# Kernel tuning notes

Hardware: AMD Instinct MI355X
Metric: run time of the kernel (lower is better)

## Reference

```python
import jax, jax.numpy as jnp
import numpy as np

D_MODEL = 1024
D_FEATURE = 64
B, S = 4, 4096


def setup_inputs() -> dict:
    key = jax.random.key(0)
    ks = jax.random.split(key, 9)
    s = 1.0 / np.sqrt(D_MODEL)
    return {
        "queries": jax.random.normal(ks[0], (B, S, D_MODEL), jnp.float32),
        "keys": jax.random.normal(ks[1], (B, S, D_MODEL), jnp.float32),
        "values": jax.random.normal(ks[2], (B, S, D_MODEL), jnp.float32),
        "Wq": jax.random.uniform(ks[3], (D_FEATURE, D_MODEL), jnp.float32, -s, s),
        "bq": jax.random.uniform(ks[4], (D_FEATURE,), jnp.float32, -s, s),
        "Wk": jax.random.uniform(ks[5], (D_FEATURE, D_MODEL), jnp.float32, -s, s),
        "bk": jax.random.uniform(ks[6], (D_FEATURE,), jnp.float32, -s, s),
        "Wv": jax.random.uniform(ks[7], (D_FEATURE, D_MODEL), jnp.float32, -s, s),
        "bv": jax.random.uniform(ks[8], (D_FEATURE,), jnp.float32, -s, s),
    }


def reference(queries, keys, values, Wq, bq, Wk, bk, Wv, bv):
    # Linear projections: x @ W.T + b
    q = jnp.einsum("bsm,fm->bsf", queries, Wq) + bq   # [B,S,Df]
    k = jnp.einsum("bsm,fm->bsf", keys, Wk) + bk
    v = jnp.einsum("bsm,fm->bsf", values, Wv) + bv
    d_k = k.shape[-1]
    # Full NxN score matrix (faithful to the naive bmm implementation)
    attn = jnp.einsum("bqf,bkf->bqk", q, k) / jnp.sqrt(jnp.float32(d_k))
    attn = jax.nn.softmax(attn, axis=2)
    # dropout is identity in eval mode; mask is never forwarded in the original
    out = jnp.einsum("bqk,bkf->bqf", attn, v)  # [B,S,Df]
    return out
```

## Files before the change

### kernel.cpp

```cpp
#include <hip/hip_runtime.h>

#define NB 4
#define SEQ 4096
#define DM 1024
#define DF 64

typedef unsigned short u16;
typedef unsigned int u32;
typedef __attribute__((ext_vector_type(8))) _Float16 half8;
typedef __attribute__((ext_vector_type(8))) unsigned short ushort8;
typedef __attribute__((ext_vector_type(4))) float f32x4;

__device__ __forceinline__ u16 f2h(float f) {
    union { _Float16 h; u16 u; } v; v.h = (_Float16)f; return v.u;
}

#define MFMAH(a, b, c) __builtin_amdgcn_mfma_f32_16x16x32_f16(a, b, c, 0, 0, 0)

__global__ __launch_bounds__(256) void wprep_kernel(
    const float* __restrict__ W0, const float* __restrict__ W1, const float* __restrict__ W2,
    u16* __restrict__ Wh)
{
    int i = blockIdx.x * 256 + threadIdx.x;
    const float* W = (i < 65536) ? W0 : (i < 131072) ? W1 : W2;
    Wh[i] = f2h(W[i & 65535]);
}

#define KST 72
__global__ __launch_bounds__(256) void proj5_kernel(
    const float* __restrict__ X0, const float* __restrict__ X1, const float* __restrict__ X2,
    const u16* __restrict__ Wh,
    const float* __restrict__ b0, const float* __restrict__ b1, const float* __restrict__ b2,
    u16* __restrict__ Oall)
{
    __shared__ u16 xs[64 * KST];
    __shared__ u16 ws[64 * KST];

    const int t    = threadIdx.x;
    const int w    = t >> 6;
    const int lane = t & 63;
    const int m15  = lane & 15;
    const int quad = lane >> 4;
    const int y    = blockIdx.y;

    const float* X    = (y == 0) ? X0 : (y == 1) ? X1 : X2;
    const float* bias = (y == 0) ? b0 : (y == 1) ? b1 : b2;
    const u16*   wp   = Wh + y * 65536;
    u16*         O    = Oall + (size_t)y * (NB * SEQ * DF);

    const long r0 = (long)blockIdx.x * 64;

    const int xrow = t >> 4;
    const int xc4  = t & 15;
    const int wrow = t >> 3;
    const int wc8  = t & 7;

    f32x4 acc[4];
#pragma unroll
    for (int F = 0; F < 4; ++F) acc[F] = (f32x4){0.f, 0.f, 0.f, 0.f};

    float4  xr[4];
    ushort8 wr[2];
#pragma unroll
    for (int i = 0; i < 4; ++i)
        xr[i] = *(const float4*)(X + (r0 + xrow + 16 * i) * DM + 4 * xc4);
#pragma unroll
    for (int i = 0; i < 2; ++i)
        wr[i] = *(const ushort8*)(wp + (wrow + 32 * i) * DM + 8 * wc8);

    for (int s = 0; s < 16; ++s) {
        __syncthreads();
#pragma unroll
        for (int i = 0; i < 4; ++i) {
            const int row = xrow + 16 * i;
            ushort4 h;
            h.x = f2h(xr[i].x); h.y = f2h(xr[i].y);
            h.z = f2h(xr[i].z); h.w = f2h(xr[i].w);
            *(ushort4*)&xs[row * KST + 4 * xc4] = h;
        }
#pragma unroll
        for (int i = 0; i < 2; ++i)
            *(ushort8*)&ws[(wrow + 32 * i) * KST + 8 * wc8] = wr[i];
        __syncthreads();

        if (s + 1 < 16) {
            const int k1 = 64 * (s + 1);
#pragma unroll
            for (int i = 0; i < 4; ++i)
                xr[i] = *(const float4*)(X + (r0 + xrow + 16 * i) * DM + k1 + 4 * xc4);
#pragma unroll
            for (int i = 0; i < 2; ++i)
                wr[i] = *(const ushort8*)(wp + (wrow + 32 * i) * DM + k1 + 8 * wc8);
        }

        const u16* ax = &xs[(16 * w + m15) * KST + quad * 8];
        half8 a0 = *(const half8*)ax;
        half8 a1 = *(const half8*)(ax + 32);
#pragma unroll
        for (int F = 0; F < 4; ++F) {
            const u16* bx = &ws[(16 * F + m15) * KST + quad * 8];
            half8 b0 = *(const half8*)bx;
            half8 b1 = *(const half8*)(bx + 32);
            acc[F] = MFMAH(a0, b0, acc[F]);
            acc[F] = MFMAH(a1, b1, acc[F]);
        }
    }

#pragma unroll
    for (int F = 0; F < 4; ++F) {
        float bv = bias[16 * F + m15];
#pragma unroll
        for (int r = 0; r < 4; ++r)
            O[(r0 + 16 * w + 4 * quad + r) * DF + 16 * F + m15] = f2h(acc[F][r] + bv);
    }
}

#define KSTR 72

__global__ __launch_bounds__(256) void attn_mfma_kernel(
    const u16* __restrict__ Qg, const u16* __restrict__ Kg, const u16* __restrict__ Vg,
    float* __restrict__ Opart, float* __restrict__ Mp, float* __restrict__ Lp,
    int ntiles, int norm)
{
    __shared__ u16 ks[64 * KSTR];
    __shared__ u16 vt[64 * KSTR];
    __shared__ u16 ps[4][16 * KSTR];

    const int t    = threadIdx.x;
    const int w    = t >> 6;
    const int lane = t & 63;
    const int m15  = lane & 15;
    const int quad = lane >> 4;
    const int b    = blockIdx.y;
    const int z    = blockIdx.z;
    const int q0   = blockIdx.x * 64;

    const u16* qptr = Qg + ((long)(b * SEQ + q0 + 16 * w + m15)) * DF + quad * 8;
    half8 qa0 = *(const half8*)qptr;
    half8 qa1 = *(const half8*)(qptr + 32);

    f32x4 accO[4];
#pragma unroll
    for (int F = 0; F < 4; ++F) accO[F] = (f32x4){0.f, 0.f, 0.f, 0.f};
    float mrow[4] = {-1e30f, -1e30f, -1e30f, -1e30f};
    float lrow[4] = {0.f, 0.f, 0.f, 0.f};

    const long kvbase = ((long)b * SEQ + (long)z * ntiles * 64) * DF;
    const ushort4* kb4 = (const ushort4*)(Kg + kvbase);
    const ushort4* vb4 = (const ushort4*)(Vg + kvbase);

    ushort4 kreg[4], vreg[4];
    const int krow  = t >> 4;
    const int kcol4 = t & 15;
    const int vj0   = (t & 15) * 4;
    const int vf0   = (t >> 4) * 4;
#pragma unroll
    for (int c = 0; c < 4; ++c) {
        kreg[c] = kb4[(krow + 16 * c) * 16 + kcol4];
        vreg[c] = vb4[(vj0 + c) * 16 + (vf0 >> 2)];
    }

    for (int tile = 0; tile < ntiles; ++tile) {
        __syncthreads();
#pragma unroll
        for (int c = 0; c < 4; ++c)
            *(ushort4*)&ks[(krow + 16 * c) * KSTR + kcol4 * 4] = kreg[c];
        {
            ushort4 w0 = {vreg[0].x, vreg[1].x, vreg[2].x, vreg[3].x};
            ushort4 w1 = {vreg[0].y, vreg[1].y, vreg[2].y, vreg[3].y};
            ushort4 w2 = {vreg[0].z, vreg[1].z, vreg[2].z, vreg[3].z};
            ushort4 w3 = {vreg[0].w, vreg[1].w, vreg[2].w, vreg[3].w};
            *(ushort4*)&vt[(vf0 + 0) * KSTR + vj0] = w0;
            *(ushort4*)&vt[(vf0 + 1) * KSTR + vj0] = w1;
            *(ushort4*)&vt[(vf0 + 2) * KSTR + vj0] = w2;
            *(ushort4*)&vt[(vf0 + 3) * KSTR + vj0] = w3;
        }
        __syncthreads();

        if (tile + 1 < ntiles) {
#pragma unroll
            for (int c = 0; c < 4; ++c) {
                kreg[c] = kb4[(tile + 1) * 1024 + (krow + 16 * c) * 16 + kcol4];
                vreg[c] = vb4[(tile + 1) * 1024 + (vj0 + c) * 16 + (vf0 >> 2)];
            }
        }

        f32x4 S[4];
#pragma unroll
        for (int T = 0; T < 4; ++T) {
            const u16* kp = &ks[(16 * T + m15) * KSTR + quad * 8];
            half8 kb0 = *(const half8*)kp;
            half8 kb1 = *(const half8*)(kp + 32);
            S[T] = MFMAH(qa0, kb0, ((f32x4){0.f, 0.f, 0.f, 0.f}));
            S[T] = MFMAH(qa1, kb1, S[T]);
        }

        float mx[4], alpha[4], mn[4], psum[4];
#pragma unroll
        for (int T = 0; T < 4; ++T)
#pragma unroll
            for (int r = 0; r < 4; ++r) S[T][r] *= 0.125f;
#pragma unroll
        for (int r = 0; r < 4; ++r) {
            mx[r] = fmaxf(fmaxf(S[0][r], S[1][r]), fmaxf(S[2][r], S[3][r]));
#pragma unroll
            for (int s = 1; s < 16; s <<= 1) mx[r] = fmaxf(mx[r], __shfl_xor(mx[r], s));
            mn[r] = fmaxf(mrow[r], mx[r]);
            alpha[r] = __expf(mrow[r] - mn[r]);
            mrow[r] = mn[r];
            psum[r] = 0.f;
        }
#pragma unroll
        for (int T = 0; T < 4; ++T)
#pragma unroll
            for (int r = 0; r < 4; ++r) {
                float p = __expf(S[T][r] - mn[r]);
                psum[r] += p;
                ps[w][(4 * quad + r) * KSTR + 16 * T + m15] = f2h(p);
            }
#pragma unroll
        for (int r = 0; r < 4; ++r) {
#pragma unroll
            for (int s = 1; s < 16; s <<= 1) psum[r] += __shfl_xor(psum[r], s);
            lrow[r] = lrow[r] * alpha[r] + psum[r];
        }
#pragma unroll
        for (int F = 0; F < 4; ++F)
#pragma unroll
            for (int r = 0; r < 4; ++r) accO[F][r] *= alpha[r];

        const u16* pp = &ps[w][m15 * KSTR + quad * 8];
        half8 pa0 = *(const half8*)pp;
        half8 pa1 = *(const half8*)(pp + 32);
#pragma unroll
        for (int F = 0; F < 4; ++F) {
            const u16* vp = &vt[(16 * F + m15) * KSTR + quad * 8];
            half8 vb0 = *(const half8*)vp;
            half8 vb1 = *(const half8*)(vp + 32);
            accO[F] = MFMAH(pa0, vb0, accO[F]);
            accO[F] = MFMAH(pa1, vb1, accO[F]);
        }
    }

    const long rowbase = (long)b * SEQ + q0 + 16 * w;
    if (norm) {
        float il[4];
#pragma unroll
        for (int r = 0; r < 4; ++r) il[r] = 1.f / lrow[r];
#pragma unroll
        for (int F = 0; F < 4; ++F)
#pragma unroll
            for (int r = 0; r < 4; ++r)
                Opart[(rowbase + 4 * quad + r) * DF + 16 * F + m15] = accO[F][r] * il[r];
    } else {
        float* Og = Opart + (size_t)z * (NB * SEQ * DF);
#pragma unroll
        for (int F = 0; F < 4; ++F)
#pragma unroll
            for (int r = 0; r < 4; ++r)
                Og[(rowbase + 4 * quad + r) * DF + 16 * F + m15] = accO[F][r];
        if (m15 == 0) {
#pragma unroll
            for (int r = 0; r < 4; ++r) {
                long rg = (long)z * (NB * SEQ) + rowbase + 4 * quad + r;
                Mp[rg] = mrow[r];
                Lp[rg] = lrow[r];
            }
        }
    }
}

__global__ __launch_bounds__(256) void combine_kernel(
    const float* __restrict__ Opart, const float* __restrict__ Mp, const float* __restrict__ Lp,
    float* __restrict__ out, int nsplit)
{
    const int tg  = blockIdx.x * 256 + threadIdx.x;
    const int row = tg >> 2;
    const int f0  = (tg & 3) * 16;

    float m = -1e30f;
    for (int g = 0; g < nsplit; ++g) m = fmaxf(m, Mp[g * (NB * SEQ) + row]);

    float l = 0.f;
    float4 o[4];
#pragma unroll
    for (int i = 0; i < 4; ++i) o[i] = (float4){0.f, 0.f, 0.f, 0.f};

    for (int g = 0; g < nsplit; ++g) {
        float e = __expf(Mp[g * (NB * SEQ) + row] - m);
        l += Lp[g * (NB * SEQ) + row] * e;
        const float* Op = Opart + ((long)g * (NB * SEQ) + row) * DF + f0;
#pragma unroll
        for (int i = 0; i < 4; ++i) {
            float4 v = *(const float4*)(Op + 4 * i);
            o[i].x += v.x * e; o[i].y += v.y * e; o[i].z += v.z * e; o[i].w += v.w * e;
        }
    }
    const float inv = 1.f / l;
#pragma unroll
    for (int i = 0; i < 4; ++i) {
        float4 v = {o[i].x * inv, o[i].y * inv, o[i].z * inv, o[i].w * inv};
        *(float4*)(out + (long)row * DF + f0 + 4 * i) = v;
    }
}

extern "C" void kernel_launch(void* const* d_in, const int* in_sizes, int n_in,
                              void* d_out, int out_size, void* d_ws, size_t ws_size,
                              hipStream_t stream) {
    (void)in_sizes; (void)n_in; (void)out_size;

    const float* X[3]  = { (const float*)d_in[0], (const float*)d_in[1], (const float*)d_in[2] };
    const float* W[3]  = { (const float*)d_in[3], (const float*)d_in[5], (const float*)d_in[7] };
    const float* Bv[3] = { (const float*)d_in[4], (const float*)d_in[6], (const float*)d_in[8] };

    char* wsb = (char*)d_ws;
    const size_t P_BYTES  = (size_t)3 * NB * SEQ * DF * 2;
    const size_t WH_BYTES = (size_t)3 * DF * DM * 2;
    const size_t ML_BYTES = (size_t)4 * NB * SEQ * 4;
    const size_t OP_BYTES = (size_t)NB * SEQ * DF * 4;

    u16*   P   = (u16*)wsb;
    u16*   Wh  = (u16*)(wsb + P_BYTES);
    float* Mp  = (float*)(wsb + P_BYTES + WH_BYTES);
    float* Lp  = (float*)(wsb + P_BYTES + WH_BYTES + ML_BYTES);
    float* Op  = (float*)(wsb + P_BYTES + WH_BYTES + 2 * ML_BYTES);
    const size_t base_need = P_BYTES + WH_BYTES + 2 * ML_BYTES;

    int nsplit = 1;
    if (ws_size >= base_need + 4 * OP_BYTES)      nsplit = 4;
    else if (ws_size >= base_need + 2 * OP_BYTES) nsplit = 2;
    const int ntiles = (SEQ / 64) / nsplit;

    float* out = (float*)d_out;

    wprep_kernel<<<768, 256, 0, stream>>>(W[0], W[1], W[2], Wh);

    dim3 pgrid(NB * SEQ / 64, 3);
    proj5_kernel<<<pgrid, 256, 0, stream>>>(X[0], X[1], X[2], Wh,
                                            Bv[0], Bv[1], Bv[2], P);

    const size_t proj_elems = (size_t)NB * SEQ * DF;
    dim3 agrid(SEQ / 64, NB, nsplit);
    if (nsplit == 1) {
        attn_mfma_kernel<<<agrid, 256, 0, stream>>>(P, P + proj_elems, P + 2 * proj_elems,
                                                    out, Mp, Lp, ntiles, 1);
    } else {
        attn_mfma_kernel<<<agrid, 256, 0, stream>>>(P, P + proj_elems, P + 2 * proj_elems,
                                                    Op, Mp, Lp, ntiles, 0);
        combine_kernel<<<(NB * SEQ * 4) / 256, 256, 0, stream>>>(Op, Mp, Lp, out, nsplit);
    }
}
```

Before: 281.7 us.

## Double-buffer projection LDS tiles and split output features across 512 threads

The projection kernel now uses two shared-memory buffers for the X and W tiles and prefetches two stages ahead, which drops one barrier per k-step. It also doubles the block to 512 threads, so eight waves split the 64 output features into two halves and each wave holds fewer accumulators. The goal is more memory parallelism and better latency hiding on what is a bandwidth-bound read of the three fp32 inputs. In exchange it doubles LDS per block and adds a launch-bounds occupancy hint that may constrain registers.

```diff
diff --git a/kernel.cpp b/kernel.cpp
--- a/kernel.cpp
+++ b/kernel.cpp
@@ -27,20 +27,22 @@
 }
 
 #define KST 72
-__global__ __launch_bounds__(256) void proj5_kernel(
+__global__ __launch_bounds__(512, 6) void proj6_kernel(
     const float* __restrict__ X0, const float* __restrict__ X1, const float* __restrict__ X2,
     const u16* __restrict__ Wh,
     const float* __restrict__ b0, const float* __restrict__ b1, const float* __restrict__ b2,
     u16* __restrict__ Oall)
 {
-    __shared__ u16 xs[64 * KST];
-    __shared__ u16 ws[64 * KST];
+    __shared__ u16 xs[2][64 * KST];
+    __shared__ u16 wt[2][64 * KST];
 
     const int t    = threadIdx.x;
     const int w    = t >> 6;
     const int lane = t & 63;
     const int m15  = lane & 15;
     const int quad = lane >> 4;
+    const int wr   = w & 3;
+    const int wf   = w >> 2;
     const int y    = blockIdx.y;
 
     const float* X    = (y == 0) ? X0 : (y == 1) ? X1 : X2;
@@ -50,68 +52,74 @@
 
     const long r0 = (long)blockIdx.x * 64;
 
-    const int xrow = t >> 4;
-    const int xc4  = t & 15;
-    const int wrow = t >> 3;
-    const int wc8  = t & 7;
-
-    f32x4 acc[4];
-#pragma unroll
-    for (int F = 0; F < 4; ++F) acc[F] = (f32x4){0.f, 0.f, 0.f, 0.f};
-
-    float4  xr[4];
-    ushort8 wr[2];
-#pragma unroll
-    for (int i = 0; i < 4; ++i)
-        xr[i] = *(const float4*)(X + (r0 + xrow + 16 * i) * DM + 4 * xc4);
-#pragma unroll
-    for (int i = 0; i < 2; ++i)
-        wr[i] = *(const ushort8*)(wp + (wrow + 32 * i) * DM + 8 * wc8);
+    const int xrow = t >> 3;
+    const int c8   = t & 7;
+
+    f32x4 acc[2];
+    acc[0] = (f32x4){0.f, 0.f, 0.f, 0.f};
+    acc[1] = (f32x4){0.f, 0.f, 0.f, 0.f};
+
+    const float* xbase = X + (r0 + xrow) * DM;
+    const u16*   wbase = wp + xrow * DM;
+
+    float4  xr2[2];
+    ushort8 wreg;
+
+    xr2[0] = *(const float4*)(xbase + 4 * c8);
+    xr2[1] = *(const float4*)(xbase + 4 * c8 + 32);
+    wreg   = *(const ushort8*)(wbase + 8 * c8);
+    {
+        ushort4 h0, h1;
+        h0.x = f2h(xr2[0].x); h0.y = f2h(xr2[0].y); h0.z = f2h(xr2[0].z); h0.w = f2h(xr2[0].w);
+        h1.x = f2h(xr2[1].x); h1.y = f2h(xr2[1].y); h1.z = f2h(xr2[1].z); h1.w = f2h(xr2[1].w);
+        *(ushort4*)&xs[0][xrow * KST + 4 * c8]      = h0;
+        *(ushort4*)&xs[0][xrow * KST + 4 * c8 + 32] = h1;
+        *(ushort8*)&wt[0][xrow * KST + 8 * c8]      = wreg;
+    }
+    xr2[0] = *(const float4*)(xbase + 64 + 4 * c8);
+    xr2[1] = *(const float4*)(xbase + 64 + 4 * c8 + 32);
+    wreg   = *(const ushort8*)(wbase + 64 + 8 * c8);
+    __syncthreads();
 
     for (int s = 0; s < 16; ++s) {
-        __syncthreads();
-#pragma unroll
-        for (int i = 0; i < 4; ++i) {
-            const int row = xrow + 16 * i;
-            ushort4 h;
-            h.x = f2h(xr[i].x); h.y = f2h(xr[i].y);
-            h.z = f2h(xr[i].z); h.w = f2h(xr[i].w);
-            *(ushort4*)&xs[row * KST + 4 * xc4] = h;
-        }
-#pragma unroll
-        for (int i = 0; i < 2; ++i)
-            *(ushort8*)&ws[(wrow + 32 * i) * KST + 8 * wc8] = wr[i];
-        __syncthreads();
+        const int cur = s & 1, nxt = cur ^ 1;
 
         if (s + 1 < 16) {
-            const int k1 = 64 * (s + 1);
-#pragma unroll
-            for (int i = 0; i < 4; ++i)
-                xr[i] = *(const float4*)(X + (r0 + xrow + 16 * i) * DM + k1 + 4 * xc4);
-#pragma unroll
-            for (int i = 0; i < 2; ++i)
-                wr[i] = *(const ushort8*)(wp + (wrow + 32 * i) * DM + k1 + 8 * wc8);
-        }
-
-        const u16* ax = &xs[(16 * w + m15) * KST + quad * 8];
+            ushort4 h0, h1;
+            h0.x = f2h(xr2[0].x); h0.y = f2h(xr2[0].y); h0.z = f2h(xr2[0].z); h0.w = f2h(xr2[0].w);
+            h1.x = f2h(xr2[1].x); h1.y = f2h(xr2[1].y); h1.z = f2h(xr2[1].z); h1.w = f2h(xr2[1].w);
+            *(ushort4*)&xs[nxt][xrow * KST + 4 * c8]      = h0;
+            *(ushort4*)&xs[nxt][xrow * KST + 4 * c8 + 32] = h1;
+            *(ushort8*)&wt[nxt][xrow * KST + 8 * c8]      = wreg;
+        }
+        if (s + 2 < 16) {
+            const int k2 = 64 * (s + 2);
+            xr2[0] = *(const float4*)(xbase + k2 + 4 * c8);
+            xr2[1] = *(const float4*)(xbase + k2 + 4 * c8 + 32);
+            wreg   = *(const ushort8*)(wbase + k2 + 8 * c8);
+        }
+
+        const u16* ax = &xs[cur][(16 * wr + m15) * KST + quad * 8];
         half8 a0 = *(const half8*)ax;
         half8 a1 = *(const half8*)(ax + 32);
 #pragma unroll
-        for (int F = 0; F < 4; ++F) {
-            const u16* bx = &ws[(16 * F + m15) * KST + quad * 8];
-            half8 b0 = *(const half8*)bx;
-            half8 b1 = *(const half8*)(bx + 32);
-            acc[F] = MFMAH(a0, b0, acc[F]);
-            acc[F] = MFMAH(a1, b1, acc[F]);
-        }
-    }
-
-#pragma unroll
-    for (int F = 0; F < 4; ++F) {
-        float bv = bias[16 * F + m15];
+        for (int Fi = 0; Fi < 2; ++Fi) {
+            const u16* bx = &wt[cur][(16 * (2 * wf + Fi) + m15) * KST + quad * 8];
+            half8 bb0 = *(const half8*)bx;
+            half8 bb1 = *(const half8*)(bx + 32);
+            acc[Fi] = MFMAH(a0, bb0, acc[Fi]);
+            acc[Fi] = MFMAH(a1, bb1, acc[Fi]);
+        }
+        __syncthreads();
+    }
+
+#pragma unroll
+    for (int Fi = 0; Fi < 2; ++Fi) {
+        const int fcol = 16 * (2 * wf + Fi) + m15;
+        float bv = bias[fcol];
 #pragma unroll
         for (int r = 0; r < 4; ++r)
-            O[(r0 + 16 * w + 4 * quad + r) * DF + 16 * F + m15] = f2h(acc[F][r] + bv);
+            O[(r0 + 16 * wr + 4 * quad + r) * DF + fcol] = f2h(acc[Fi][r] + bv);
     }
 }
 
@@ -336,7 +344,7 @@
     wprep_kernel<<<768, 256, 0, stream>>>(W[0], W[1], W[2], Wh);
 
     dim3 pgrid(NB * SEQ / 64, 3);
-    proj5_kernel<<<pgrid, 256, 0, stream>>>(X[0], X[1], X[2], Wh,
+    proj6_kernel<<<pgrid, 512, 0, stream>>>(X[0], X[1], X[2], Wh,
                                             Bv[0], Bv[1], Bv[2], P);
 
     const size_t proj_elems = (size_t)NB * SEQ * DF;
```

Result: no change. 280.9 us (-0.3%).

## Load projection activations directly from global into MFMA registers, stage only weights

Applied to the files above, without the earlier changes.

The projection kernel no longer stages X tiles through LDS. Each lane reads its fp32 activation row slice straight from global memory and converts it to fp16 in registers for the MFMA A operand. Only the weight matrix is staged in LDS, in larger 256-wide K chunks with register prefetch, which cuts the number of barriers per block. The cost is uncoalesced-ish per-lane global loads of X with no software prefetch, so latency hiding now depends on occupancy, for which a launch-bounds hint is added.

```diff
diff --git a/kernel.cpp b/kernel.cpp
--- a/kernel.cpp
+++ b/kernel.cpp
@@ -26,15 +26,14 @@
     Wh[i] = f2h(W[i & 65535]);
 }
 
-#define KST 72
-__global__ __launch_bounds__(256) void proj5_kernel(
+#define WSTR 264
+__global__ __launch_bounds__(256, 3) void proj7_kernel(
     const float* __restrict__ X0, const float* __restrict__ X1, const float* __restrict__ X2,
     const u16* __restrict__ Wh,
     const float* __restrict__ b0, const float* __restrict__ b1, const float* __restrict__ b2,
     u16* __restrict__ Oall)
 {
-    __shared__ u16 xs[64 * KST];
-    __shared__ u16 ws[64 * KST];
+    __shared__ u16 wlds[64 * WSTR];
 
     const int t    = threadIdx.x;
     const int w    = t >> 6;
@@ -49,60 +48,49 @@
     u16*         O    = Oall + (size_t)y * (NB * SEQ * DF);
 
     const long r0 = (long)blockIdx.x * 64;
-
-    const int xrow = t >> 4;
-    const int xc4  = t & 15;
-    const int wrow = t >> 3;
-    const int wc8  = t & 7;
+    const float* xrow = X + (r0 + 16 * w + m15) * DM;
+
+    const int wr2 = t >> 5;
+    const int wc  = (t & 31) * 8;
 
     f32x4 acc[4];
 #pragma unroll
     for (int F = 0; F < 4; ++F) acc[F] = (f32x4){0.f, 0.f, 0.f, 0.f};
 
-    float4  xr[4];
-    ushort8 wr[2];
-#pragma unroll
-    for (int i = 0; i < 4; ++i)
-        xr[i] = *(const float4*)(X + (r0 + xrow + 16 * i) * DM + 4 * xc4);
-#pragma unroll
-    for (int i = 0; i < 2; ++i)
-        wr[i] = *(const ushort8*)(wp + (wrow + 32 * i) * DM + 8 * wc8);
-
-    for (int s = 0; s < 16; ++s) {
+    ushort8 wreg[8];
+#pragma unroll
+    for (int i = 0; i < 8; ++i)
+        wreg[i] = *(const ushort8*)(wp + (i * 8 + wr2) * DM + wc);
+
+    for (int c = 0; c < 4; ++c) {
+        const int k0 = c * 256;
         __syncthreads();
 #pragma unroll
-        for (int i = 0; i < 4; ++i) {
-            const int row = xrow + 16 * i;
-            ushort4 h;
-            h.x = f2h(xr[i].x); h.y = f2h(xr[i].y);
-            h.z = f2h(xr[i].z); h.w = f2h(xr[i].w);
-            *(ushort4*)&xs[row * KST + 4 * xc4] = h;
-        }
-#pragma unroll
-        for (int i = 0; i < 2; ++i)
-            *(ushort8*)&ws[(wrow + 32 * i) * KST + 8 * wc8] = wr[i];
+        for (int i = 0; i < 8; ++i)
+            *(ushort8*)&wlds[(i * 8 + wr2) * WSTR + wc] = wreg[i];
         __syncthreads();
 
-        if (s + 1 < 16) {
-            const int k1 = 64 * (s + 1);
-#pragma unroll
-            for (int i = 0; i < 4; ++i)
-                xr[i] = *(const float4*)(X + (r0 + xrow + 16 * i) * DM + k1 + 4 * xc4);
-#pragma unroll
-            for (int i = 0; i < 2; ++i)
-                wr[i] = *(const ushort8*)(wp + (wrow + 32 * i) * DM + k1 + 8 * wc8);
-        }
-
-        const u16* ax = &xs[(16 * w + m15) * KST + quad * 8];
-        half8 a0 = *(const half8*)ax;
-        half8 a1 = *(const half8*)(ax + 32);
-#pragma unroll
-        for (int F = 0; F < 4; ++F) {
-            const u16* bx = &ws[(16 * F + m15) * KST + quad * 8];
-            half8 b0 = *(const half8*)bx;
-            half8 b1 = *(const half8*)(bx + 32);
-            acc[F] = MFMAH(a0, b0, acc[F]);
-            acc[F] = MFMAH(a1, b1, acc[F]);
+        if (c + 1 < 4) {
+#pragma unroll
+            for (int i = 0; i < 8; ++i)
+                wreg[i] = *(const ushort8*)(wp + (i * 8 + wr2) * DM + k0 + 256 + wc);
+        }
+
+#pragma unroll
+        for (int s = 0; s < 8; ++s) {
+            const int kk = 32 * s + quad * 8;
+            float4 x0 = *(const float4*)(xrow + k0 + kk);
+            float4 x1 = *(const float4*)(xrow + k0 + kk + 4);
+            half8 a;
+            a[0] = (_Float16)x0.x; a[1] = (_Float16)x0.y;
+            a[2] = (_Float16)x0.z; a[3] = (_Float16)x0.w;
+            a[4] = (_Float16)x1.x; a[5] = (_Float16)x1.y;
+            a[6] = (_Float16)x1.z; a[7] = (_Float16)x1.w;
+#pragma unroll
+            for (int F = 0; F < 4; ++F) {
+                half8 b = *(const half8*)&wlds[(16 * F + m15) * WSTR + kk];
+                acc[F] = MFMAH(a, b, acc[F]);
+            }
         }
     }
 
@@ -336,7 +324,7 @@
     wprep_kernel<<<768, 256, 0, stream>>>(W[0], W[1], W[2], Wh);
 
     dim3 pgrid(NB * SEQ / 64, 3);
-    proj5_kernel<<<pgrid, 256, 0, stream>>>(X[0], X[1], X[2], Wh,
+    proj7_kernel<<<pgrid, 256, 0, stream>>>(X[0], X[1], X[2], Wh,
                                             Bv[0], Bv[1], Bv[2], P);
 
     const size_t proj_elems = (size_t)NB * SEQ * DF;
```

After: 281.7 us. About the same (-0.0%).
